# Kernel optimization log

Hardware: AMD Instinct MI355X
Metric: run time of the kernel (lower is better)

Reference implementation:

```python
import jax, jax.numpy as jnp
import numpy as np

EMB = 768
HEADS = 3
HD = EMB // HEADS  # 256
B, S = 4, 2048


def setup_inputs() -> dict:
    key = jax.random.key(0)
    ks = jax.random.split(key, 8)
    inputs_for_keys = jax.random.normal(ks[0], (B, S, EMB), dtype=jnp.float32)
    inputs_for_values = jax.random.normal(ks[1], (B, S, EMB), dtype=jnp.float32)
    inputs_for_queries = jax.random.normal(ks[2], (B, S, EMB), dtype=jnp.float32)
    # stacked per-head projection weights: [heads, emb, head_dim]
    # original uses 'random_uniform' init (small uniform); scale ~0.05
    Wk = jax.random.uniform(ks[3], (HEADS, EMB, HD), jnp.float32, -0.05, 0.05)
    Wv = jax.random.uniform(ks[4], (HEADS, EMB, HD), jnp.float32, -0.05, 0.05)
    Wq = jax.random.uniform(ks[5], (HEADS, EMB, HD), jnp.float32, -0.05, 0.05)
    Wo = jax.random.normal(ks[6], (EMB, EMB), dtype=jnp.float32) * (1.0 / np.sqrt(EMB))
    bo = jnp.zeros((EMB,), dtype=jnp.float32)
    return {
        "inputs_for_keys": inputs_for_keys,
        "inputs_for_values": inputs_for_values,
        "inputs_for_queries": inputs_for_queries,
        "Wk": Wk, "Wv": Wv, "Wq": Wq, "Wo": Wo, "bo": bo,
    }


def reference(inputs_for_keys, inputs_for_values, inputs_for_queries, Wk, Wv, Wq, Wo, bo):
    # per-head projections, batched over heads: [b, h, s, f]
    K = jnp.einsum('bse,hef->bhsf', inputs_for_keys, Wk)
    V = jnp.einsum('bse,hef->bhsf', inputs_for_values, Wv)
    Q = jnp.einsum('bse,hef->bhsf', inputs_for_queries, Wq)

    seq_k = inputs_for_keys.shape[1]
    seq_q = inputs_for_queries.shape[1]
    # NOTE: original scales by sqrt(window_size_keys) (seq len), not sqrt(d_k)
    scale = jnp.sqrt(jnp.float32(seq_k))

    scores = jnp.einsum('bhqf,bhkf->bhqk', Q, K) / scale
    # causal mask: -inf strictly above the diagonal (j > i)
    mask = jnp.triu(jnp.full((seq_q, seq_k), -jnp.inf, dtype=scores.dtype), k=1)
    scores = scores + mask

    attn = jax.nn.softmax(scores, axis=-1)  # [b,h,q,k]
    heads = jnp.einsum('bhqk,bhkf->bhqf', attn, V)

    # concat heads along feature dim: [b, q, heads*hd]
    b, h, q, f = heads.shape
    concat = heads.transpose(0, 2, 1, 3).reshape(b, q, h * f)
    return concat @ Wo + bo
```

## Files before the change

### kernel.cpp

```cpp
#include <hip/hip_runtime.h>

#define BATCH 4
#define NHEADS 3
#define SEQ 2048
#define HDIM 256
#define EMBD 768
#define MTOT (BATCH*SEQ)
#define WSZ (NHEADS*EMBD*HDIM)

typedef unsigned short u16x8 __attribute__((ext_vector_type(8)));
typedef unsigned short u16x4 __attribute__((ext_vector_type(4)));
typedef __bf16 bf16x8 __attribute__((ext_vector_type(8)));
typedef float fx4 __attribute__((ext_vector_type(4)));

__device__ __forceinline__ unsigned short f2bf(float x) {
    union { float f; unsigned int u; } v; v.f = x;
    unsigned int r = v.u + 0x7fffu + ((v.u >> 16) & 1u);
    return (unsigned short)(r >> 16);
}

__device__ __forceinline__ fx4 mfma16(u16x8 a, u16x8 b, fx4 c) {
    return __builtin_amdgcn_mfma_f32_16x16x32_bf16(
        __builtin_bit_cast(bf16x8, a), __builtin_bit_cast(bf16x8, b), c, 0, 0, 0);
}

__device__ __forceinline__ void gl_lds16(const unsigned short* g, unsigned short* l) {
    __builtin_amdgcn_global_load_lds(
        (const __attribute__((address_space(1))) unsigned int*)g,
        (__attribute__((address_space(3))) unsigned int*)l, 16, 0, 0);
}

__device__ const unsigned char attn_sched[48] = {
    124,125, 63, 120,121, 116,117, 59, 112,113, 108,109, 55, 104,105,
    100,101, 51,  96, 97,  92, 93, 47,  88, 89,  84, 85, 43,  80, 81,
     76, 77, 39,  72, 73,  68, 69, 35,  64, 65,  31, 27, 23, 19, 15,
     11,  7,  3
};

__global__ __launch_bounds__(256) void castAw_kernel(
    const float* __restrict__ Ak, const float* __restrict__ Av,
    const float* __restrict__ Aq,
    const float* __restrict__ Wk, const float* __restrict__ Wv,
    const float* __restrict__ Wq, const float* __restrict__ Wo,
    unsigned short* __restrict__ Abf, unsigned short* __restrict__ Wt,
    unsigned short* __restrict__ Wot)
{
    __shared__ float tile[64][65];
    int bx = blockIdx.x;
    if (bx < 9216) {
        int e = (bx * 256 + threadIdx.x) * 8;
        int t = e / (MTOT * EMBD);
        int r = e - t * (MTOT * EMBD);
        const float* A = (t == 0) ? Ak : (t == 1) ? Av : Aq;
        const fx4* s = (const fx4*)(A + r);
        fx4 v0 = s[0], v1 = s[1];
        u16x8 o;
        o[0]=f2bf(v0[0]); o[1]=f2bf(v0[1]); o[2]=f2bf(v0[2]); o[3]=f2bf(v0[3]);
        o[4]=f2bf(v1[0]); o[5]=f2bf(v1[1]); o[6]=f2bf(v1[2]); o[7]=f2bf(v1[3]);
        *(u16x8*)(Abf + e) = o;
        return;
    }
    int z = bx - 9216;
    const float* src; unsigned short* dst;
    int src_ld, dst_ld, e0, f0;
    if (z < 432) {
        int t = z / 144, rem = z - t * 144;
        int h = rem / 48, tl = rem - h * 48;
        e0 = (tl % 12) * 64; f0 = (tl / 12) * 64;
        const float* W = (t == 0) ? Wk : (t == 1) ? Wv : Wq;
        src = W + h * 768 * 256; src_ld = 256;
        dst = Wt + t * WSZ + h * 256 * 768; dst_ld = 768;
    } else {
        int zz = z - 432;
        e0 = (zz % 12) * 64; f0 = (zz / 12) * 64;
        src = Wo; src_ld = 768;
        dst = Wot; dst_ld = 768;
    }
    int tx = threadIdx.x & 63, ty4 = threadIdx.x >> 6;
    #pragma unroll
    for (int i = 0; i < 16; ++i) {
        int r = ty4 + i * 4;
        tile[r][tx] = src[(e0 + r) * src_ld + f0 + tx];
    }
    __syncthreads();
    #pragma unroll
    for (int i = 0; i < 16; ++i) {
        int r = ty4 + i * 4;
        dst[(f0 + r) * dst_ld + e0 + tx] = f2bf(tile[tx][r]);
    }
}

__global__ __launch_bounds__(256, 3) void proj_kernel(
    const unsigned short* __restrict__ Abf, const unsigned short* __restrict__ Wt,
    unsigned short* __restrict__ Kg, unsigned short* __restrict__ Vg,
    unsigned short* __restrict__ Qg)
{
    __shared__ alignas(16) unsigned short Bs[24576];

    int z = blockIdx.z;
    const unsigned short* A = Abf + z * (MTOT * EMBD);
    int m0 = blockIdx.x * 256;
    int nb = blockIdx.y;
    int h = nb >> 2, fbase = (nb & 3) * 64;
    const unsigned short* W = Wt + z * WSZ + (h * 256 + fbase) * EMBD;

    int tid = threadIdx.x;
    int w = tid >> 6, ln = tid & 63;
    int lane16 = ln & 15, quad = ln >> 4;
    int mw = w * 64;

    fx4 acc[4][4];
    #pragma unroll
    for (int i = 0; i < 4; ++i)
        #pragma unroll
        for (int j = 0; j < 4; ++j) acc[i][j] = (fx4){0.f, 0.f, 0.f, 0.f};

    const unsigned short* Ap = A + (m0 + mw + lane16) * EMBD + quad * 8;

    u16x8 afc[4], afn[4];
    #pragma unroll
    for (int i = 0; i < 4; ++i) afc[i] = *(const u16x8*)(Ap + i * 16 * EMBD);

    int bsw = lane16 & 7;

    #pragma unroll
    for (int ph = 0; ph < 2; ++ph) {
        __syncthreads();
        #pragma unroll
        for (int jj = 0; jj < 12; ++jj) {
            int U = jj * 256 + tid;
            int row = U / 48;
            int slot = U - row * 48;
            int gu = (slot & ~7) | ((slot & 7) ^ (row & 7));
            gl_lds16(W + row * EMBD + ph * 384 + gu * 8, &Bs[U * 8]);
        }
        __syncthreads();

        #pragma unroll
        for (int kk = 0; kk < 12; ++kk) {
            int kbn = ph * 384 + kk * 32 + 32;
            if (kbn < EMBD) {
                #pragma unroll
                for (int i = 0; i < 4; ++i)
                    afn[i] = *(const u16x8*)(Ap + i * 16 * EMBD + kbn);
            }
            #pragma unroll
            for (int j = 0; j < 4; ++j) {
                int u = kk * 4 + quad;
                int slot = (u & ~7) | ((u & 7) ^ bsw);
                u16x8 bf = *(const u16x8*)&Bs[((j * 16 + lane16) * 48 + slot) * 8];
                #pragma unroll
                for (int i = 0; i < 4; ++i)
                    acc[i][j] = mfma16(afc[i], bf, acc[i][j]);
            }
            if (kbn < EMBD) {
                #pragma unroll
                for (int i = 0; i < 4; ++i) afc[i] = afn[i];
            }
        }
    }

    int b = m0 >> 11, sq0 = m0 & 2047;

    if (z == 1) {
        __syncthreads();
        #pragma unroll
        for (int i = 0; i < 4; ++i)
            #pragma unroll
            for (int j = 0; j < 4; ++j) {
                int fl = j * 16 + lane16;
                int ml = mw + i * 16 + quad * 4;
                u16x4 pk;
                pk[0] = f2bf(acc[i][j][0]); pk[1] = f2bf(acc[i][j][1]);
                pk[2] = f2bf(acc[i][j][2]); pk[3] = f2bf(acc[i][j][3]);
                *(u16x4*)&Bs[fl * 264 + ml] = pk;
            }
        __syncthreads();
        int fl = tid >> 2, seg = (tid & 3) * 64;
        const unsigned short* sp = &Bs[fl * 264 + seg];
        unsigned short* dp = Vg + ((size_t)(b * NHEADS + h) * HDIM + fbase + fl) * SEQ
                           + sq0 + seg;
        #pragma unroll
        for (int c = 0; c < 8; ++c)
            *(u16x8*)(dp + c * 8) = *(const u16x8*)(sp + c * 8);
    } else {
        unsigned short* dst0 = (z == 0) ? Kg : Qg;
        #pragma unroll
        for (int q = 0; q < 2; ++q) {
            __syncthreads();
            #pragma unroll
            for (int i = 0; i < 4; ++i)
                #pragma unroll
                for (int j2 = 0; j2 < 2; ++j2) {
                    int jj = q * 2 + j2;
                    int row = mw + i * 16 + quad * 4;
                    int col = j2 * 16 + lane16;
                    #pragma unroll
                    for (int r = 0; r < 4; ++r)
                        Bs[(row + r) * 40 + col] = f2bf(acc[i][jj][r]);
                }
            __syncthreads();
            const unsigned short* sp = &Bs[tid * 40];
            unsigned short* dp = dst0 + ((size_t)(b * NHEADS + h) * SEQ + sq0 + tid) * HDIM
                               + fbase + q * 32;
            #pragma unroll
            for (int c = 0; c < 4; ++c)
                *(u16x8*)(dp + c * 8) = *(const u16x8*)(sp + c * 8);
        }
    }
}

__global__ __launch_bounds__(256) void attn_kernel(
    const unsigned short* __restrict__ Kg, const unsigned short* __restrict__ Vg,
    const unsigned short* __restrict__ Qg, unsigned short* __restrict__ heads,
    float* __restrict__ Opart, float* __restrict__ Lpart)
{
    __shared__ alignas(16) unsigned short Ks[64 * 256];
    __shared__ alignas(16) unsigned short Vs[256 * 64];

    int bx = blockIdx.x;
    int bh = bx % 12;
    int ent = attn_sched[bx / 12];
    int qt = ent >> 2, kc = ent & 3;
    int tid = threadIdx.x;
    int w = tid >> 6, ln = tid & 63;
    int lane16 = ln & 15, quad = ln >> 4;
    int q0w = qt * 64 + w * 16;

    const unsigned short* Kbase = Kg + bh * (SEQ * HDIM);
    const unsigned short* Vbase = Vg + bh * (SEQ * HDIM);
    const unsigned short* Qbase = Qg + bh * (SEQ * HDIM);

    u16x8 qf[8];
    {
        const unsigned short* qrow = Qbase + (q0w + lane16) * HDIM + quad * 8;
        #pragma unroll
        for (int c = 0; c < 8; ++c) qf[c] = *(const u16x8*)(qrow + c * 32);
    }

    fx4 o[16];
    #pragma unroll
    for (int i = 0; i < 16; ++i) o[i] = (fx4){0.f, 0.f, 0.f, 0.f};
    float lsum = 0.f;

    const float Cs2 = 0.03188010519640429f;

    int t0, t1;
    if (kc == 3) { t0 = 0; t1 = qt + 1; }
    else         { int half = (qt + 1) >> 1;
                   t0 = kc ? half : 0; t1 = kc ? qt + 1 : half; }

    const unsigned short* kgp = Kbase + (tid >> 5) * HDIM
                              + (((tid & 31) ^ (tid >> 5)) * 8);
    const unsigned short* vgp = Vbase + (tid >> 3) * SEQ
                              + (((tid & 7) ^ ((tid >> 3) & 7)) * 8);
    unsigned short* ksl = &Ks[tid * 8];
    unsigned short* vsl = &Vs[tid * 8];

    int ksw = lane16 & 7;

    for (int kt = t0; kt < t1; ++kt) {
        int k0 = kt * 64;
        __syncthreads();
        #pragma unroll
        for (int j = 0; j < 8; ++j)
            gl_lds16(kgp + (k0 + j * 8) * HDIM, ksl + j * 2048);
        #pragma unroll
        for (int j = 0; j < 8; ++j)
            gl_lds16(vgp + j * 32 * SEQ + k0, vsl + j * 2048);
        __syncthreads();

        fx4 sacc[4];
        #pragma unroll
        for (int ks = 0; ks < 4; ++ks) sacc[ks] = (fx4){0.f,0.f,0.f,0.f};
        #pragma unroll
        for (int c = 0; c < 8; ++c) {
            #pragma unroll
            for (int ks = 0; ks < 4; ++ks) {
                u16x8 kf = *(const u16x8*)&Ks[(ks * 16 + lane16) * 256
                                              + (((c * 4 + quad) ^ ksw) << 3)];
                sacc[ks] = mfma16(kf, qf[c], sacc[ks]);
            }
        }

        float p[4][4];
        int q = q0w + lane16;
        #pragma unroll
        for (int ks = 0; ks < 4; ++ks)
            #pragma unroll
            for (int r = 0; r < 4; ++r) {
                int ka_ = k0 + ks * 16 + quad * 4 + r;
                float e = exp2f(sacc[ks][r] * Cs2);
                p[ks][r] = (ka_ <= q) ? e : 0.f;
                lsum += p[ks][r];
            }

        #pragma unroll
        for (int hh = 0; hh < 2; ++hh) {
            u16x8 pf;
            #pragma unroll
            for (int j = 0; j < 8; ++j) {
                int srcLane = ((((quad << 1) + (j >> 2)) & 3) << 4) | lane16;
                float v0 = __shfl(p[2 * hh][j & 3], srcLane, 64);
                float v1 = __shfl(p[2 * hh + 1][j & 3], srcLane, 64);
                pf[j] = f2bf(quad >= 2 ? v1 : v0);
            }
            #pragma unroll
            for (int ft = 0; ft < 16; ++ft) {
                u16x8 vf = *(const u16x8*)&Vs[(ft * 16 + lane16) * 64
                                              + (((hh * 4 + quad) ^ ksw) << 3)];
                o[ft] = mfma16(pf, vf, o[ft]);
            }
        }
    }

    lsum += __shfl_xor(lsum, 16, 64);
    lsum += __shfl_xor(lsum, 32, 64);

    if (kc == 3) {
        float linv = 1.f / lsum;
        float inv[4];
        #pragma unroll
        for (int r = 0; r < 4; ++r) inv[r] = __shfl(linv, quad * 4 + r, 64);
        int b = bh / 3, h = bh - (bh / 3) * 3;
        unsigned short* hp = heads + (b * SEQ + q0w + quad * 4) * EMBD + h * HDIM + lane16;
        #pragma unroll
        for (int ft = 0; ft < 16; ++ft)
            #pragma unroll
            for (int r = 0; r < 4; ++r)
                hp[r * EMBD + ft * 16] = f2bf(o[ft][r] * inv[r]);
    } else {
        int slot = (bh * 16 + (qt - 16)) * 2 + kc;
        float* Op = Opart + slot * 16384 + (w * 16 + quad * 4) * 256 + lane16;
        #pragma unroll
        for (int ft = 0; ft < 16; ++ft)
            #pragma unroll
            for (int r = 0; r < 4; ++r)
                Op[r * 256 + ft * 16] = o[ft][r];
        if (quad == 0) Lpart[slot * 64 + w * 16 + lane16] = lsum;
    }
}

__global__ __launch_bounds__(256) void combine_kernel(
    const float* __restrict__ Opart, const float* __restrict__ Lpart,
    unsigned short* __restrict__ heads)
{
    int t = blockIdx.x;
    int bh = t >> 4, qt = (t & 15) + 16;
    int s0 = t * 2, s1 = s0 + 1;
    int tid = threadIdx.x;
    int row = tid >> 2, fseg = (tid & 3) * 64;
    float l = Lpart[s0 * 64 + row] + Lpart[s1 * 64 + row];
    float inv = 1.f / l;
    const fx4* O0 = (const fx4*)(Opart + s0 * 16384 + row * 256 + fseg);
    const fx4* O1 = (const fx4*)(Opart + s1 * 16384 + row * 256 + fseg);
    int b = bh / 3, h = bh - (bh / 3) * 3;
    unsigned short* hp = heads + (b * SEQ + qt * 64 + row) * EMBD + h * HDIM + fseg;
    #pragma unroll
    for (int i = 0; i < 16; ++i) {
        fx4 v = O0[i] + O1[i];
        u16x4 pk;
        pk[0] = f2bf(v[0] * inv); pk[1] = f2bf(v[1] * inv);
        pk[2] = f2bf(v[2] * inv); pk[3] = f2bf(v[3] * inv);
        *(u16x4*)(hp + i * 4) = pk;
    }
}

__global__ __launch_bounds__(256, 3) void outproj_kernel(
    const unsigned short* __restrict__ A, const unsigned short* __restrict__ Wot,
    const float* __restrict__ bo, float* __restrict__ out)
{
    __shared__ alignas(16) unsigned short Bs[24576];

    int m0 = blockIdx.x * 256;
    int nb = blockIdx.y;
    const unsigned short* W = Wot + (nb * 64) * EMBD;

    int tid = threadIdx.x;
    int w = tid >> 6, ln = tid & 63;
    int lane16 = ln & 15, quad = ln >> 4;
    int mw = w * 64;

    fx4 acc[4][4];
    #pragma unroll
    for (int i = 0; i < 4; ++i)
        #pragma unroll
        for (int j = 0; j < 4; ++j) acc[i][j] = (fx4){0.f, 0.f, 0.f, 0.f};

    const unsigned short* Ap = A + (m0 + mw + lane16) * EMBD + quad * 8;

    u16x8 afc[4], afn[4];
    #pragma unroll
    for (int i = 0; i < 4; ++i) afc[i] = *(const u16x8*)(Ap + i * 16 * EMBD);

    int bsw = lane16 & 7;

    #pragma unroll
    for (int ph = 0; ph < 2; ++ph) {
        __syncthreads();
        #pragma unroll
        for (int jj = 0; jj < 12; ++jj) {
            int U = jj * 256 + tid;
            int row = U / 48;
            int slot = U - row * 48;
            int gu = (slot & ~7) | ((slot & 7) ^ (row & 7));
            gl_lds16(W + row * EMBD + ph * 384 + gu * 8, &Bs[U * 8]);
        }
        __syncthreads();

        #pragma unroll
        for (int kk = 0; kk < 12; ++kk) {
            int kbn = ph * 384 + kk * 32 + 32;
            if (kbn < EMBD) {
                #pragma unroll
                for (int i = 0; i < 4; ++i)
                    afn[i] = *(const u16x8*)(Ap + i * 16 * EMBD + kbn);
            }
            #pragma unroll
            for (int j = 0; j < 4; ++j) {
                int u = kk * 4 + quad;
                int slot = (u & ~7) | ((u & 7) ^ bsw);
                u16x8 bf = *(const u16x8*)&Bs[((j * 16 + lane16) * 48 + slot) * 8];
                #pragma unroll
                for (int i = 0; i < 4; ++i)
                    acc[i][j] = mfma16(afc[i], bf, acc[i][j]);
            }
            if (kbn < EMBD) {
                #pragma unroll
                for (int i = 0; i < 4; ++i) afc[i] = afn[i];
            }
        }
    }

    #pragma unroll
    for (int j = 0; j < 4; ++j) {
        int n = nb * 64 + j * 16 + lane16;
        float bias = bo[n];
        #pragma unroll
        for (int i = 0; i < 4; ++i) {
            int mb = m0 + mw + i * 16 + quad * 4;
            #pragma unroll
            for (int r = 0; r < 4; ++r)
                out[(size_t)(mb + r) * EMBD + n] = acc[i][j][r] + bias;
        }
    }
}

extern "C" void kernel_launch(void* const* d_in, const int* in_sizes, int n_in,
                              void* d_out, int out_size, void* d_ws, size_t ws_size,
                              hipStream_t stream) {
    const float* Ak = (const float*)d_in[0];
    const float* Av = (const float*)d_in[1];
    const float* Aq = (const float*)d_in[2];
    const float* Wk = (const float*)d_in[3];
    const float* Wv = (const float*)d_in[4];
    const float* Wq = (const float*)d_in[5];
    const float* Wo = (const float*)d_in[6];
    const float* bo = (const float*)d_in[7];
    float* out = (float*)d_out;

    char* base = (char*)d_ws;
    unsigned short* Wt    = (unsigned short*)(base);
    unsigned short* Wot   = (unsigned short*)(base + 3538944);
    unsigned short* Abf   = (unsigned short*)(base + 4718592);
    unsigned short* Kg    = (unsigned short*)(base + 42467328);
    unsigned short* Vg    = (unsigned short*)(base + 55050240);
    unsigned short* Qg    = (unsigned short*)(base + 67633152);
    unsigned short* heads = (unsigned short*)(base + 80216064);
    float* Opart = (float*)(base + 4718592);
    float* Lpart = (float*)(base + 4718592 + 25165824);

    castAw_kernel<<<dim3(9792), dim3(256), 0, stream>>>(
        Ak, Av, Aq, Wk, Wv, Wq, Wo, Abf, Wt, Wot);
    proj_kernel<<<dim3(32, 12, 3), dim3(256), 0, stream>>>(
        Abf, Wt, Kg, Vg, Qg);
    attn_kernel<<<dim3(576), dim3(256), 0, stream>>>(
        Kg, Vg, Qg, heads, Opart, Lpart);
    combine_kernel<<<dim3(192), dim3(256), 0, stream>>>(Opart, Lpart, heads);
    outproj_kernel<<<dim3(32, 12), dim3(256), 0, stream>>>(heads, Wot, bo, out);
}
```

Before: 307.1 us.

## Fuse fp32-to-bf16 activation cast into projection GEMM and retile over full heads

Removes the separate activation cast pass, which wrote a bf16 copy of all three input tensors. The projection kernel now reads fp32 activations directly, converts them to bf16 and stores them in LDS. The projection is also retiled to 64 rows by a full 256-wide head per block, with weights streamed from global into registers. This saves one full read/write round trip of the activations, but each activation tile is now re-read in fp32 by three head blocks and the weights are read from global without LDS sharing.

```diff
diff --git a/kernel.cpp b/kernel.cpp
--- a/kernel.cpp
+++ b/kernel.cpp
@@ -37,30 +37,13 @@
      11,  7,  3
 };
 
-__global__ __launch_bounds__(256) void castAw_kernel(
-    const float* __restrict__ Ak, const float* __restrict__ Av,
-    const float* __restrict__ Aq,
+__global__ __launch_bounds__(256) void castW_kernel(
     const float* __restrict__ Wk, const float* __restrict__ Wv,
     const float* __restrict__ Wq, const float* __restrict__ Wo,
-    unsigned short* __restrict__ Abf, unsigned short* __restrict__ Wt,
-    unsigned short* __restrict__ Wot)
+    unsigned short* __restrict__ Wt, unsigned short* __restrict__ Wot)
 {
     __shared__ float tile[64][65];
-    int bx = blockIdx.x;
-    if (bx < 9216) {
-        int e = (bx * 256 + threadIdx.x) * 8;
-        int t = e / (MTOT * EMBD);
-        int r = e - t * (MTOT * EMBD);
-        const float* A = (t == 0) ? Ak : (t == 1) ? Av : Aq;
-        const fx4* s = (const fx4*)(A + r);
-        fx4 v0 = s[0], v1 = s[1];
-        u16x8 o;
-        o[0]=f2bf(v0[0]); o[1]=f2bf(v0[1]); o[2]=f2bf(v0[2]); o[3]=f2bf(v0[3]);
-        o[4]=f2bf(v1[0]); o[5]=f2bf(v1[1]); o[6]=f2bf(v1[2]); o[7]=f2bf(v1[3]);
-        *(u16x8*)(Abf + e) = o;
-        return;
-    }
-    int z = bx - 9216;
+    int z = blockIdx.x;
     const float* src; unsigned short* dst;
     int src_ld, dst_ld, e0, f0;
     if (z < 432) {
@@ -91,23 +74,22 @@
 }
 
 __global__ __launch_bounds__(256, 3) void proj_kernel(
-    const unsigned short* __restrict__ Abf, const unsigned short* __restrict__ Wt,
+    const float* __restrict__ Ak, const float* __restrict__ Av,
+    const float* __restrict__ Aq, const unsigned short* __restrict__ Wt,
     unsigned short* __restrict__ Kg, unsigned short* __restrict__ Vg,
     unsigned short* __restrict__ Qg)
 {
-    __shared__ alignas(16) unsigned short Bs[24576];
+    __shared__ alignas(16) unsigned short S[24576];
 
     int z = blockIdx.z;
-    const unsigned short* A = Abf + z * (MTOT * EMBD);
-    int m0 = blockIdx.x * 256;
-    int nb = blockIdx.y;
-    int h = nb >> 2, fbase = (nb & 3) * 64;
-    const unsigned short* W = Wt + z * WSZ + (h * 256 + fbase) * EMBD;
+    const float* A = (z == 0) ? Ak : (z == 1) ? Av : Aq;
+    int m0 = blockIdx.x * 64;
+    int h = blockIdx.y;
+    const unsigned short* W = Wt + z * WSZ + (h * 256) * EMBD;
 
     int tid = threadIdx.x;
     int w = tid >> 6, ln = tid & 63;
     int lane16 = ln & 15, quad = ln >> 4;
-    int mw = w * 64;
 
     fx4 acc[4][4];
     #pragma unroll
@@ -115,98 +97,101 @@
         #pragma unroll
         for (int j = 0; j < 4; ++j) acc[i][j] = (fx4){0.f, 0.f, 0.f, 0.f};
 
-    const unsigned short* Ap = A + (m0 + mw + lane16) * EMBD + quad * 8;
-
-    u16x8 afc[4], afn[4];
-    #pragma unroll
-    for (int i = 0; i < 4; ++i) afc[i] = *(const u16x8*)(Ap + i * 16 * EMBD);
-
-    int bsw = lane16 & 7;
-
-    #pragma unroll
-    for (int ph = 0; ph < 2; ++ph) {
-        __syncthreads();
-        #pragma unroll
-        for (int jj = 0; jj < 12; ++jj) {
-            int U = jj * 256 + tid;
-            int row = U / 48;
-            int slot = U - row * 48;
-            int gu = (slot & ~7) | ((slot & 7) ^ (row & 7));
-            gl_lds16(W + row * EMBD + ph * 384 + gu * 8, &Bs[U * 8]);
-        }
-        __syncthreads();
-
-        #pragma unroll
-        for (int kk = 0; kk < 12; ++kk) {
-            int kbn = ph * 384 + kk * 32 + 32;
-            if (kbn < EMBD) {
-                #pragma unroll
-                for (int i = 0; i < 4; ++i)
-                    afn[i] = *(const u16x8*)(Ap + i * 16 * EMBD + kbn);
-            }
+    const unsigned short* Bp = W + (w * 64 + lane16) * EMBD + quad * 8;
+
+    u16x8 bfc[4], bfn[4];
+    #pragma unroll
+    for (int j = 0; j < 4; ++j)
+        bfc[j] = *(const u16x8*)(Bp + j * 16 * EMBD);
+
+    int lsw = lane16 & 7;
+
+    #pragma unroll
+    for (int it = 0; it < 24; ++it) {
+        if ((it % 12) == 0) {
+            int ph = it / 12;
+            __syncthreads();
+            #pragma unroll
+            for (int jj = 0; jj < 12; ++jj) {
+                int U = jj * 256 + tid;
+                int row = U / 48;
+                int slot = U - row * 48;
+                int gu = (slot & ~7) | ((slot & 7) ^ (row & 7));
+                const float* src = A + (size_t)(m0 + row) * EMBD + ph * 384 + gu * 8;
+                fx4 v0 = *(const fx4*)(src);
+                fx4 v1 = *(const fx4*)(src + 4);
+                u16x8 o;
+                o[0]=f2bf(v0[0]); o[1]=f2bf(v0[1]); o[2]=f2bf(v0[2]); o[3]=f2bf(v0[3]);
+                o[4]=f2bf(v1[0]); o[5]=f2bf(v1[1]); o[6]=f2bf(v1[2]); o[7]=f2bf(v1[3]);
+                *(u16x8*)&S[U * 8] = o;
+            }
+            __syncthreads();
+        }
+        int kk = it % 12;
+        if (it + 1 < 24) {
+            int k0n = (it + 1) * 32;
+            #pragma unroll
+            for (int j = 0; j < 4; ++j)
+                bfn[j] = *(const u16x8*)(Bp + j * 16 * EMBD + k0n);
+        }
+        int u = kk * 4 + quad;
+        int uS = (u & ~7) | ((u & 7) ^ lsw);
+        u16x8 af[4];
+        #pragma unroll
+        for (int i = 0; i < 4; ++i)
+            af[i] = *(const u16x8*)&S[((i * 16 + lane16) * 48 + uS) * 8];
+        #pragma unroll
+        for (int j = 0; j < 4; ++j)
+            #pragma unroll
+            for (int i = 0; i < 4; ++i)
+                acc[i][j] = mfma16(af[i], bfc[j], acc[i][j]);
+        if (it + 1 < 24) {
+            #pragma unroll
+            for (int j = 0; j < 4; ++j) bfc[j] = bfn[j];
+        }
+    }
+
+    int b = m0 >> 11, sq0 = m0 & 2047;
+
+    if (z == 1) {
+        __syncthreads();
+        #pragma unroll
+        for (int i = 0; i < 4; ++i)
             #pragma unroll
             for (int j = 0; j < 4; ++j) {
-                int u = kk * 4 + quad;
-                int slot = (u & ~7) | ((u & 7) ^ bsw);
-                u16x8 bf = *(const u16x8*)&Bs[((j * 16 + lane16) * 48 + slot) * 8];
-                #pragma unroll
-                for (int i = 0; i < 4; ++i)
-                    acc[i][j] = mfma16(afc[i], bf, acc[i][j]);
-            }
-            if (kbn < EMBD) {
-                #pragma unroll
-                for (int i = 0; i < 4; ++i) afc[i] = afn[i];
-            }
-        }
-    }
-
-    int b = m0 >> 11, sq0 = m0 & 2047;
-
-    if (z == 1) {
-        __syncthreads();
-        #pragma unroll
-        for (int i = 0; i < 4; ++i)
-            #pragma unroll
-            for (int j = 0; j < 4; ++j) {
-                int fl = j * 16 + lane16;
-                int ml = mw + i * 16 + quad * 4;
+                int fl = w * 64 + j * 16 + lane16;
+                int ml = i * 16 + quad * 4;
                 u16x4 pk;
                 pk[0] = f2bf(acc[i][j][0]); pk[1] = f2bf(acc[i][j][1]);
                 pk[2] = f2bf(acc[i][j][2]); pk[3] = f2bf(acc[i][j][3]);
-                *(u16x4*)&Bs[fl * 264 + ml] = pk;
-            }
-        __syncthreads();
-        int fl = tid >> 2, seg = (tid & 3) * 64;
-        const unsigned short* sp = &Bs[fl * 264 + seg];
-        unsigned short* dp = Vg + ((size_t)(b * NHEADS + h) * HDIM + fbase + fl) * SEQ
-                           + sq0 + seg;
+                *(u16x4*)&S[fl * 72 + ml] = pk;
+            }
+        __syncthreads();
+        const unsigned short* sp = &S[tid * 72];
+        unsigned short* dp = Vg + ((size_t)(b * NHEADS + h) * HDIM + tid) * SEQ + sq0;
         #pragma unroll
         for (int c = 0; c < 8; ++c)
             *(u16x8*)(dp + c * 8) = *(const u16x8*)(sp + c * 8);
     } else {
+        __syncthreads();
+        #pragma unroll
+        for (int i = 0; i < 4; ++i)
+            #pragma unroll
+            for (int j = 0; j < 4; ++j) {
+                int fl = w * 64 + j * 16 + lane16;
+                int ml = i * 16 + quad * 4;
+                #pragma unroll
+                for (int r = 0; r < 4; ++r)
+                    S[(ml + r) * 264 + fl] = f2bf(acc[i][j][r]);
+            }
+        __syncthreads();
         unsigned short* dst0 = (z == 0) ? Kg : Qg;
-        #pragma unroll
-        for (int q = 0; q < 2; ++q) {
-            __syncthreads();
-            #pragma unroll
-            for (int i = 0; i < 4; ++i)
-                #pragma unroll
-                for (int j2 = 0; j2 < 2; ++j2) {
-                    int jj = q * 2 + j2;
-                    int row = mw + i * 16 + quad * 4;
-                    int col = j2 * 16 + lane16;
-                    #pragma unroll
-                    for (int r = 0; r < 4; ++r)
-                        Bs[(row + r) * 40 + col] = f2bf(acc[i][jj][r]);
-                }
-            __syncthreads();
-            const unsigned short* sp = &Bs[tid * 40];
-            unsigned short* dp = dst0 + ((size_t)(b * NHEADS + h) * SEQ + sq0 + tid) * HDIM
-                               + fbase + q * 32;
-            #pragma unroll
-            for (int c = 0; c < 4; ++c)
-                *(u16x8*)(dp + c * 8) = *(const u16x8*)(sp + c * 8);
-        }
+        int ml = tid >> 2, fseg = (tid & 3) * 64;
+        const unsigned short* sp = &S[ml * 264 + fseg];
+        unsigned short* dp = dst0 + ((size_t)(b * NHEADS + h) * SEQ + sq0 + ml) * HDIM + fseg;
+        #pragma unroll
+        for (int c = 0; c < 8; ++c)
+            *(u16x8*)(dp + c * 8) = *(const u16x8*)(sp + c * 8);
     }
 }
 
@@ -462,18 +447,17 @@
     char* base = (char*)d_ws;
     unsigned short* Wt    = (unsigned short*)(base);
     unsigned short* Wot   = (unsigned short*)(base + 3538944);
-    unsigned short* Abf   = (unsigned short*)(base + 4718592);
+    float* Opart          = (float*)(base + 4718592);
+    float* Lpart          = (float*)(base + 4718592 + 25165824);
     unsigned short* Kg    = (unsigned short*)(base + 42467328);
     unsigned short* Vg    = (unsigned short*)(base + 55050240);
     unsigned short* Qg    = (unsigned short*)(base + 67633152);
     unsigned short* heads = (unsigned short*)(base + 80216064);
-    float* Opart = (float*)(base + 4718592);
-    float* Lpart = (float*)(base + 4718592 + 25165824);
-
-    castAw_kernel<<<dim3(9792), dim3(256), 0, stream>>>(
-        Ak, Av, Aq, Wk, Wv, Wq, Wo, Abf, Wt, Wot);
-    proj_kernel<<<dim3(32, 12, 3), dim3(256), 0, stream>>>(
-        Abf, Wt, Kg, Vg, Qg);
+
+    castW_kernel<<<dim3(576), dim3(256), 0, stream>>>(
+        Wk, Wv, Wq, Wo, Wt, Wot);
+    proj_kernel<<<dim3(128, 3, 3), dim3(256), 0, stream>>>(
+        Ak, Av, Aq, Wt, Kg, Vg, Qg);
     attn_kernel<<<dim3(576), dim3(256), 0, stream>>>(
         Kg, Vg, Qg, heads, Opart, Lpart);
     combine_kernel<<<dim3(192), dim3(256), 0, stream>>>(Opart, Lpart, heads);
```

Result: slower. 319.5 us (+4.1%).
